# Performance work log

Hardware: AMD Instinct MI355X
Metric: run time of the kernel (lower is better)

## Reference

```python
import jax, jax.numpy as jnp
import numpy as np


def setup_inputs() -> dict:
    key = jax.random.key(0)
    kq, kk, kv = jax.random.split(key, 3)
    N, L, H, D = 2, 2048, 16, 64
    Q = jax.random.normal(kq, (N, L, H, D), dtype=jnp.float32)
    K = jax.random.normal(kk, (N, L, H, D), dtype=jnp.float32)
    V = jax.random.normal(kv, (N, L, H, D), dtype=jnp.float32)
    return {"Q": Q, "K": K, "V": V}


def reference(Q, K, V):
    # Q: [N, l_q, H, d], K: [N, l_k, H, d], V: [N, l_k, H, d_v]
    d_key = K.shape[-1]
    scale = 1.0 / jnp.sqrt(jnp.asarray(d_key, dtype=Q.dtype))
    # scores: [N, l_q, l_k, H] (matches torch sum over d, softmax over l_k)
    scores = jnp.einsum("nqhd,nkhd->nqkh", Q, K) * scale
    attn = jax.nn.softmax(scores, axis=2)
    # out: [N, l_q, H, d_v]
    out = jnp.einsum("nqkh,nkhd->nqhd", attn, V)
    return out
```

## Files before the change

### kernel.cpp

```cpp
#include <hip/hip_runtime.h>
#include <hip/hip_bf16.h>

typedef __attribute__((ext_vector_type(8))) short bf16x8;
typedef __attribute__((ext_vector_type(4))) float float4_t;
typedef __attribute__((ext_vector_type(2))) float f32x2;
typedef __attribute__((ext_vector_type(16))) float f32x16;
typedef __attribute__((ext_vector_type(4))) int int4v;
typedef __attribute__((ext_vector_type(2))) int int2v;
typedef __attribute__((ext_vector_type(4))) unsigned uint4v;

constexpr int Lseq = 2048;
constexpr int ROWS = 1024;
constexpr int KB   = 64;
constexpr float SCALE_LOG2E = 0.18033688011112042f;
constexpr float THR = 8.0f;

__device__ __forceinline__ int cvtpk(float lo, float hi) {
  int r; asm("v_cvt_pk_bf16_f32 %0, %1, %2" : "=v"(r) : "v"(lo), "v"(hi)); return r;
}
__device__ __forceinline__ f32x2 pkadd(f32x2 a, f32x2 b) {
  f32x2 r; asm("v_pk_add_f32 %0, %1, %2" : "=v"(r) : "v"(a), "v"(b)); return r;
}
__device__ __forceinline__ void plswap(int& a, int& b) {
  int2v r = __builtin_amdgcn_permlane32_swap(a, b, false, false);
  a = r[0]; b = r[1];
}
__device__ __forceinline__ float mx3(float a, float b, float c) {
  return fmaxf(fmaxf(a, b), c);
}
__device__ __forceinline__ int4v pk8(float4_t a, float4_t b) {
  int4v t;
  t[0] = cvtpk(a[0], a[1]); t[1] = cvtpk(a[2], a[3]);
  t[2] = cvtpk(b[0], b[1]); t[3] = cvtpk(b[2], b[3]);
  return t;
}
__device__ __forceinline__ uint4v make_srsrc(const void* p) {
  unsigned long long a = (unsigned long long)p;
  uint4v r; r[0] = (unsigned)a; r[1] = (unsigned)(a >> 32) & 0xffffu;
  r[2] = 0xffffffffu; r[3] = 0x00020000u;
  return r;
}
__device__ __forceinline__ float blds(unsigned voff, uint4v rs, int soff) {
  float d;
  asm volatile("buffer_load_dword %0, %1, %2, %3 offen"
               : "=v"(d) : "v"(voff), "s"(rs), "s"(soff));
  return d;
}

#define MFMA32(A, B, C) __builtin_amdgcn_mfma_f32_32x32x16_bf16((A), (B), (C), 0, 0, 0)

__global__ __launch_bounds__(256, 2)
void attn_fwd(const float* __restrict__ Qg, const float* __restrict__ Kg,
              const float* __restrict__ Vg, float* __restrict__ Og) {
  __shared__ __align__(16) short kv_lds[2][2][KB * 64];

  int wg  = blockIdx.x;
  int swz = (wg & 7) * 64 + (wg >> 3);
  int nh  = swz >> 4;
  int qt  = swz & 15;
  const size_t base = (size_t)(nh >> 4) * Lseq * ROWS + (size_t)(nh & 15) * 64;

  const int tid  = threadIdx.x;
  const int lane = tid & 63;
  const int wid  = tid >> 6;
  const int lq   = lane & 31;
  const int hi   = lane >> 5;

  bf16x8 qf[4];
  {
    const float* qrow = Qg + base + (size_t)(qt * 128 + wid * 32 + lq) * ROWS + hi * 8;
#pragma unroll
    for (int c = 0; c < 4; ++c) {
      float4_t a = *(const float4_t*)(qrow + c * 16);
      float4_t b = *(const float4_t*)(qrow + c * 16 + 4);
#pragma unroll
      for (int j = 0; j < 4; ++j) { a[j] *= SCALE_LOG2E; b[j] *= SCALE_LOG2E; }
      qf[c] = __builtin_bit_cast(bf16x8, pk8(a, b));
    }
  }

  const uint4v rsK = make_srsrc(Kg + base);
  const uint4v rsV = make_srsrc(Vg + base);
  unsigned voffk  = (unsigned)(((tid >> 2) * ROWS + (tid & 3) * 16) * 4);
  unsigned voffv  = (unsigned)((((tid >> 6) * 8) * ROWS + (tid & 63)) * 4);
  unsigned voffv2 = voffv + 131072u;

  const int krow = tid >> 2;
  const int kwb  = krow * 128 + (tid & 3) * 32;
  const int kswz = (krow & 7) << 4;
  const int kb0  = kwb ^ kswz, kb1 = (kwb + 16) ^ kswz;
  const int vd   = tid & 63;
  const int vwb  = vd * 128 + (tid >> 6) * 16;
  const int vswz = (vd & 7) << 4;
  const int vb0  = vwb ^ vswz, vb1 = (vwb + 64) ^ vswz;
  const int rsw = (lq & 7) << 4;
  const int rb0 = lq * 128 + hi * 16;
  const int rb1 = (32 + lq) * 128 + hi * 16;

  float4_t kr[4]; float vr[16];
  auto stage_issue = [&]() {
    asm volatile(
        "buffer_load_dwordx4 %0, %4, %5, 0 offen\n\t"
        "buffer_load_dwordx4 %1, %4, %5, 0 offen offset:16\n\t"
        "buffer_load_dwordx4 %2, %4, %5, 0 offen offset:32\n\t"
        "buffer_load_dwordx4 %3, %4, %5, 0 offen offset:48"
        : "=v"(kr[0]), "=v"(kr[1]), "=v"(kr[2]), "=v"(kr[3])
        : "v"(voffk), "s"(rsK));
#pragma unroll
    for (int j = 0; j < 8; ++j) {
      vr[j]     = blds(voffv,  rsV, j * 4096);
      vr[8 + j] = blds(voffv2, rsV, j * 4096);
    }
    voffk += 262144u; voffv += 262144u; voffv2 += 262144u;
  };
  auto stage_write = [&](int buf) {
    asm volatile("s_waitcnt vmcnt(0)"
                 : "+v"(kr[0]), "+v"(kr[1]), "+v"(kr[2]), "+v"(kr[3]),
                   "+v"(vr[0]), "+v"(vr[1]), "+v"(vr[2]), "+v"(vr[3]),
                   "+v"(vr[4]), "+v"(vr[5]), "+v"(vr[6]), "+v"(vr[7]),
                   "+v"(vr[8]), "+v"(vr[9]), "+v"(vr[10]), "+v"(vr[11]),
                   "+v"(vr[12]), "+v"(vr[13]), "+v"(vr[14]), "+v"(vr[15]));
    char* kdst = (char*)&kv_lds[buf][0][0];
    *(int4v*)(kdst + kb0) = pk8(kr[0], kr[1]);
    *(int4v*)(kdst + kb1) = pk8(kr[2], kr[3]);
    char* vdst = (char*)&kv_lds[buf][1][0];
    int4v w0, w1;
    w0[0] = cvtpk(vr[0], vr[1]);   w0[1] = cvtpk(vr[2], vr[3]);
    w0[2] = cvtpk(vr[4], vr[5]);   w0[3] = cvtpk(vr[6], vr[7]);
    w1[0] = cvtpk(vr[8], vr[9]);   w1[1] = cvtpk(vr[10], vr[11]);
    w1[2] = cvtpk(vr[12], vr[13]); w1[3] = cvtpk(vr[14], vr[15]);
    *(int4v*)(vdst + vb0) = w0;
    *(int4v*)(vdst + vb1) = w1;
  };

  float m = 0.f, l = 0.f;
  f32x16 acc0, acc1;
#pragma unroll
  for (int r = 0; r < 16; ++r) { acc0[r] = 0.f; acc1[r] = 0.f; }

  stage_issue();
  stage_write(0);
  __syncthreads();

  int cur = 0;
  for (int kt = 0; kt < Lseq; kt += KB) {
    const bool more = (kt + KB) < Lseq;
    if (more) stage_issue();

    f32x16 s0, s1;
#pragma unroll
    for (int r = 0; r < 16; ++r) { s0[r] = -m; s1[r] = -m; }
    const char* kld = (const char*)&kv_lds[cur][0][0];
#pragma unroll
    for (int c = 0; c < 4; ++c) {
      bf16x8 ka = *(const bf16x8*)(kld + ((rb0 + c * 32) ^ rsw));
      s0 = MFMA32(ka, qf[c], s0);
    }
#pragma unroll
    for (int c = 0; c < 4; ++c) {
      bf16x8 ka = *(const bf16x8*)(kld + ((rb1 + c * 32) ^ rsw));
      s1 = MFMA32(ka, qf[c], s1);
    }

    float w0 = mx3(s0[0], s0[1], s0[2]);
    float w1 = mx3(s0[3], s0[4], s0[5]);
    float w2 = mx3(s0[6], s0[7], s0[8]);
    float w3 = mx3(s0[9], s0[10], s0[11]);
    float w4 = mx3(s0[12], s0[13], s0[14]);
    float w5 = mx3(s0[15], s1[0], s1[1]);
    float w6 = mx3(s1[2], s1[3], s1[4]);
    float w7 = mx3(s1[5], s1[6], s1[7]);
    float w8 = mx3(s1[8], s1[9], s1[10]);
    float w9 = mx3(s1[11], s1[12], s1[13]);
    float wa = fmaxf(s1[14], s1[15]);
    float x0 = mx3(w0, w1, w2);
    float x1 = mx3(w3, w4, w5);
    float x2 = mx3(w6, w7, w8);
    float x3 = mx3(w9, wa, x2);
    float pm = mx3(x0, x1, x3);
    {
      int a = __float_as_int(pm), b = a;
      plswap(a, b);
      pm = fmaxf(__int_as_float(a), __int_as_float(b));
    }

    if (__all(pm <= THR)) {
#pragma unroll
      for (int r = 0; r < 16; ++r) {
        s0[r] = __builtin_amdgcn_exp2f(s0[r]);
        s1[r] = __builtin_amdgcn_exp2f(s1[r]);
      }
    } else {
      float mn = fmaxf(pm, 0.f);
      m += mn;
      float f = __builtin_amdgcn_exp2f(-mn);
      l *= f;
#pragma unroll
      for (int r = 0; r < 16; ++r) {
        int qr = (r & 3) + 8 * (r >> 2) + 4 * hi;
        float fq = __shfl(f, qr);
        acc0[r] *= fq; acc1[r] *= fq;
      }
#pragma unroll
      for (int r = 0; r < 16; ++r) {
        s0[r] = __builtin_amdgcn_exp2f(s0[r] - mn);
        s1[r] = __builtin_amdgcn_exp2f(s1[r] - mn);
      }
    }

#define S2(v, i) (f32x2{(v)[2 * (i)], (v)[2 * (i) + 1]})
    {
      f32x2 u0 = pkadd(S2(s0, 0), S2(s0, 1));
      f32x2 u1 = pkadd(S2(s0, 2), S2(s0, 3));
      f32x2 u2 = pkadd(S2(s0, 4), S2(s0, 5));
      f32x2 u3 = pkadd(S2(s0, 6), S2(s0, 7));
      f32x2 u4 = pkadd(S2(s1, 0), S2(s1, 1));
      f32x2 u5 = pkadd(S2(s1, 2), S2(s1, 3));
      f32x2 u6 = pkadd(S2(s1, 4), S2(s1, 5));
      f32x2 u7 = pkadd(S2(s1, 6), S2(s1, 7));
      u0 = pkadd(u0, u1); u2 = pkadd(u2, u3);
      u4 = pkadd(u4, u5); u6 = pkadd(u6, u7);
      u0 = pkadd(u0, u2); u4 = pkadd(u4, u6);
      u0 = pkadd(u0, u4);
      float rs = u0[0] + u0[1];
      int a = __float_as_int(rs), b = a;
      plswap(a, b);
      l += __int_as_float(a) + __int_as_float(b);
    }
#undef S2

    bf16x8 pa[4];
#pragma unroll
    for (int c = 0; c < 4; ++c) {
      const f32x16& sv = (c < 2) ? s0 : s1;
      const int br = (c & 1) * 8;
      int t0 = cvtpk(sv[br + 0], sv[br + 1]);
      int t1 = cvtpk(sv[br + 2], sv[br + 3]);
      int t2 = cvtpk(sv[br + 4], sv[br + 5]);
      int t3 = cvtpk(sv[br + 6], sv[br + 7]);
      plswap(t0, t2);
      plswap(t1, t3);
      int4v t; t[0] = t0; t[1] = t1; t[2] = t2; t[3] = t3;
      pa[c] = __builtin_bit_cast(bf16x8, t);
    }

    const char* vld = (const char*)&kv_lds[cur][1][0];
#pragma unroll
    for (int c = 0; c < 4; ++c) {
      bf16x8 vb = *(const bf16x8*)(vld + ((rb0 + c * 32) ^ rsw));
      acc0 = MFMA32(pa[c], vb, acc0);
    }
#pragma unroll
    for (int c = 0; c < 4; ++c) {
      bf16x8 vb = *(const bf16x8*)(vld + ((rb1 + c * 32) ^ rsw));
      acc1 = MFMA32(pa[c], vb, acc1);
    }

    if (more) stage_write(cur ^ 1);
    __syncthreads();
    cur ^= 1;
  }

  float linv = 1.0f / l;
#pragma unroll
  for (int r = 0; r < 16; ++r) {
    int qr = (r & 3) + 8 * (r >> 2) + 4 * hi;
    float li = __shfl(linv, qr);
    float* orow = Og + base + (size_t)(qt * 128 + wid * 32 + qr) * ROWS;
    orow[lq]      = acc0[r] * li;
    orow[32 + lq] = acc1[r] * li;
  }
}

extern "C" void kernel_launch(void* const* d_in, const int* in_sizes, int n_in,
                              void* d_out, int out_size, void* d_ws, size_t ws_size,
                              hipStream_t stream) {
  const float* Q = (const float*)d_in[0];
  const float* K = (const float*)d_in[1];
  const float* V = (const float*)d_in[2];
  float* O = (float*)d_out;
  attn_fwd<<<dim3(512), dim3(256), 0, stream>>>(Q, K, V, O);
}
```

Measured before the change: 65.79 us.

## Pre-convert K/V to swizzled bf16 images and DMA them directly into LDS

Adds a preconv kernel that converts K and V to bf16 once per call, pre-swizzled into the exact LDS tile layout, and writes them to global scratch buffers. The attention kernel then streams those tiles straight into LDS with global_load_lds, so the per-workgroup fp32 loads, packing and LDS writes disappear. Workgroups shrink to 128 threads covering 64 query rows, doubling the grid. The cost is a second launch plus the round trip through the global scratch buffers, and each workgroup now loads K/V for only 64 query rows, so K/V reuse per workgroup halves.

```diff
diff --git a/kernel.cpp b/kernel.cpp
--- a/kernel.cpp
+++ b/kernel.cpp
@@ -7,13 +7,14 @@
 typedef __attribute__((ext_vector_type(16))) float f32x16;
 typedef __attribute__((ext_vector_type(4))) int int4v;
 typedef __attribute__((ext_vector_type(2))) int int2v;
-typedef __attribute__((ext_vector_type(4))) unsigned uint4v;
 
 constexpr int Lseq = 2048;
 constexpr int ROWS = 1024;
-constexpr int KB   = 64;
 constexpr float SCALE_LOG2E = 0.18033688011112042f;
 constexpr float THR = 8.0f;
+
+__device__ short g_Kb[32 * 32 * 4096];
+__device__ short g_Vb[32 * 32 * 4096];
 
 __device__ __forceinline__ int cvtpk(float lo, float hi) {
   int r; asm("v_cvt_pk_bf16_f32 %0, %1, %2" : "=v"(r) : "v"(lo), "v"(hi)); return r;
@@ -34,30 +35,63 @@
   t[2] = cvtpk(b[0], b[1]); t[3] = cvtpk(b[2], b[3]);
   return t;
 }
-__device__ __forceinline__ uint4v make_srsrc(const void* p) {
-  unsigned long long a = (unsigned long long)p;
-  uint4v r; r[0] = (unsigned)a; r[1] = (unsigned)(a >> 32) & 0xffffu;
-  r[2] = 0xffffffffu; r[3] = 0x00020000u;
-  return r;
-}
-__device__ __forceinline__ float blds(unsigned voff, uint4v rs, int soff) {
-  float d;
-  asm volatile("buffer_load_dword %0, %1, %2, %3 offen"
-               : "=v"(d) : "v"(voff), "s"(rs), "s"(soff));
-  return d;
+__device__ __forceinline__ void dma16(const void* g, void* l) {
+  __builtin_amdgcn_global_load_lds(
+      (const __attribute__((address_space(1))) void*)g,
+      (__attribute__((address_space(3))) void*)l, 16, 0, 0);
 }
 
 #define MFMA32(A, B, C) __builtin_amdgcn_mfma_f32_32x32x16_bf16((A), (B), (C), 0, 0, 0)
 
-__global__ __launch_bounds__(256, 2)
-void attn_fwd(const float* __restrict__ Qg, const float* __restrict__ Kg,
-              const float* __restrict__ Vg, float* __restrict__ Og) {
-  __shared__ __align__(16) short kv_lds[2][2][KB * 64];
-
-  int wg  = blockIdx.x;
-  int swz = (wg & 7) * 64 + (wg >> 3);
-  int nh  = swz >> 4;
-  int qt  = swz & 15;
+__global__ __launch_bounds__(256)
+void preconv(const float* __restrict__ Kg, const float* __restrict__ Vg) {
+  const int bid = blockIdx.x;
+  const int nh = bid >> 5;
+  const int kt = bid & 31;
+  const size_t base = (size_t)(nh >> 4) * Lseq * ROWS + (size_t)(nh & 15) * 64;
+  const int tid = threadIdx.x;
+  char* kimg = (char*)g_Kb + ((size_t)nh * 32 + kt) * 8192;
+  char* vimg = (char*)g_Vb + ((size_t)nh * 32 + kt) * 8192;
+
+  {
+    const int row = tid >> 2;
+    const float* src = Kg + base + (size_t)(kt * 64 + row) * ROWS + (tid & 3) * 16;
+    float4_t a = ((const float4_t*)src)[0];
+    float4_t b = ((const float4_t*)src)[1];
+    float4_t c = ((const float4_t*)src)[2];
+    float4_t d = ((const float4_t*)src)[3];
+    const int swz = (row & 7) << 4;
+    const int wb  = row * 128 + (tid & 3) * 32;
+    *(int4v*)(kimg + (wb ^ swz))        = pk8(a, b);
+    *(int4v*)(kimg + ((wb + 16) ^ swz)) = pk8(c, d);
+  }
+  {
+    const int d0 = tid & 63;
+    const int lb = tid >> 6;
+    const float* src = Vg + base + (size_t)(kt * 64 + lb * 16) * ROWS + d0;
+    float v[16];
+#pragma unroll
+    for (int j = 0; j < 16; ++j) v[j] = src[(size_t)j * ROWS];
+    int4v w0, w1;
+    w0[0] = cvtpk(v[0], v[1]);   w0[1] = cvtpk(v[2], v[3]);
+    w0[2] = cvtpk(v[4], v[5]);   w0[3] = cvtpk(v[6], v[7]);
+    w1[0] = cvtpk(v[8], v[9]);   w1[1] = cvtpk(v[10], v[11]);
+    w1[2] = cvtpk(v[12], v[13]); w1[3] = cvtpk(v[14], v[15]);
+    const int swz = (d0 & 7) << 4;
+    const int wb  = d0 * 128 + lb * 32;
+    *(int4v*)(vimg + (wb ^ swz))        = w0;
+    *(int4v*)(vimg + ((wb + 16) ^ swz)) = w1;
+  }
+}
+
+__global__ __launch_bounds__(128, 2)
+void attn_fwd(const float* __restrict__ Qg, float* __restrict__ Og) {
+  __shared__ __align__(16) short kv_lds[2][2][64 * 64];
+
+  const int wg  = blockIdx.x;
+  const int swz = (wg & 7) * 128 + (wg >> 3);
+  const int nh  = swz >> 5;
+  const int qt  = swz & 31;
   const size_t base = (size_t)(nh >> 4) * Lseq * ROWS + (size_t)(nh & 15) * 64;
 
   const int tid  = threadIdx.x;
@@ -68,7 +102,7 @@
 
   bf16x8 qf[4];
   {
-    const float* qrow = Qg + base + (size_t)(qt * 128 + wid * 32 + lq) * ROWS + hi * 8;
+    const float* qrow = Qg + base + (size_t)(qt * 64 + wid * 32 + lq) * ROWS + hi * 8;
 #pragma unroll
     for (int c = 0; c < 4; ++c) {
       float4_t a = *(const float4_t*)(qrow + c * 16);
@@ -79,73 +113,31 @@
     }
   }
 
-  const uint4v rsK = make_srsrc(Kg + base);
-  const uint4v rsV = make_srsrc(Vg + base);
-  unsigned voffk  = (unsigned)(((tid >> 2) * ROWS + (tid & 3) * 16) * 4);
-  unsigned voffv  = (unsigned)((((tid >> 6) * 8) * ROWS + (tid & 63)) * 4);
-  unsigned voffv2 = voffv + 131072u;
-
-  const int krow = tid >> 2;
-  const int kwb  = krow * 128 + (tid & 3) * 32;
-  const int kswz = (krow & 7) << 4;
-  const int kb0  = kwb ^ kswz, kb1 = (kwb + 16) ^ kswz;
-  const int vd   = tid & 63;
-  const int vwb  = vd * 128 + (tid >> 6) * 16;
-  const int vswz = (vd & 7) << 4;
-  const int vb0  = vwb ^ vswz, vb1 = (vwb + 64) ^ vswz;
+  const char* gsrc = (const char*)(wid == 0 ? g_Kb : g_Vb) + (size_t)nh * (32 * 8192)
+                     + lane * 16;
+  auto stage = [&](int buf, int t) {
+    const char* s = gsrc + (size_t)t * 8192;
+    char* d = (char*)&kv_lds[buf][wid][0];
+#pragma unroll
+    for (int i = 0; i < 8; ++i) dma16(s + i * 1024, d + i * 1024);
+  };
+
   const int rsw = (lq & 7) << 4;
   const int rb0 = lq * 128 + hi * 16;
   const int rb1 = (32 + lq) * 128 + hi * 16;
 
-  float4_t kr[4]; float vr[16];
-  auto stage_issue = [&]() {
-    asm volatile(
-        "buffer_load_dwordx4 %0, %4, %5, 0 offen\n\t"
-        "buffer_load_dwordx4 %1, %4, %5, 0 offen offset:16\n\t"
-        "buffer_load_dwordx4 %2, %4, %5, 0 offen offset:32\n\t"
-        "buffer_load_dwordx4 %3, %4, %5, 0 offen offset:48"
-        : "=v"(kr[0]), "=v"(kr[1]), "=v"(kr[2]), "=v"(kr[3])
-        : "v"(voffk), "s"(rsK));
-#pragma unroll
-    for (int j = 0; j < 8; ++j) {
-      vr[j]     = blds(voffv,  rsV, j * 4096);
-      vr[8 + j] = blds(voffv2, rsV, j * 4096);
-    }
-    voffk += 262144u; voffv += 262144u; voffv2 += 262144u;
-  };
-  auto stage_write = [&](int buf) {
-    asm volatile("s_waitcnt vmcnt(0)"
-                 : "+v"(kr[0]), "+v"(kr[1]), "+v"(kr[2]), "+v"(kr[3]),
-                   "+v"(vr[0]), "+v"(vr[1]), "+v"(vr[2]), "+v"(vr[3]),
-                   "+v"(vr[4]), "+v"(vr[5]), "+v"(vr[6]), "+v"(vr[7]),
-                   "+v"(vr[8]), "+v"(vr[9]), "+v"(vr[10]), "+v"(vr[11]),
-                   "+v"(vr[12]), "+v"(vr[13]), "+v"(vr[14]), "+v"(vr[15]));
-    char* kdst = (char*)&kv_lds[buf][0][0];
-    *(int4v*)(kdst + kb0) = pk8(kr[0], kr[1]);
-    *(int4v*)(kdst + kb1) = pk8(kr[2], kr[3]);
-    char* vdst = (char*)&kv_lds[buf][1][0];
-    int4v w0, w1;
-    w0[0] = cvtpk(vr[0], vr[1]);   w0[1] = cvtpk(vr[2], vr[3]);
-    w0[2] = cvtpk(vr[4], vr[5]);   w0[3] = cvtpk(vr[6], vr[7]);
-    w1[0] = cvtpk(vr[8], vr[9]);   w1[1] = cvtpk(vr[10], vr[11]);
-    w1[2] = cvtpk(vr[12], vr[13]); w1[3] = cvtpk(vr[14], vr[15]);
-    *(int4v*)(vdst + vb0) = w0;
-    *(int4v*)(vdst + vb1) = w1;
-  };
-
   float m = 0.f, l = 0.f;
   f32x16 acc0, acc1;
 #pragma unroll
   for (int r = 0; r < 16; ++r) { acc0[r] = 0.f; acc1[r] = 0.f; }
 
-  stage_issue();
-  stage_write(0);
+  stage(0, 0);
+  asm volatile("s_waitcnt vmcnt(0)" ::: "memory");
   __syncthreads();
 
   int cur = 0;
-  for (int kt = 0; kt < Lseq; kt += KB) {
-    const bool more = (kt + KB) < Lseq;
-    if (more) stage_issue();
+  for (int t = 0; t < 32; ++t) {
+    if (t < 31) stage(cur ^ 1, t + 1);
 
     f32x16 s0, s1;
 #pragma unroll
@@ -240,8 +232,8 @@
       int t3 = cvtpk(sv[br + 6], sv[br + 7]);
       plswap(t0, t2);
       plswap(t1, t3);
-      int4v t; t[0] = t0; t[1] = t1; t[2] = t2; t[3] = t3;
-      pa[c] = __builtin_bit_cast(bf16x8, t);
+      int4v tt; tt[0] = t0; tt[1] = t1; tt[2] = t2; tt[3] = t3;
+      pa[c] = __builtin_bit_cast(bf16x8, tt);
     }
 
     const char* vld = (const char*)&kv_lds[cur][1][0];
@@ -256,7 +248,7 @@
       acc1 = MFMA32(pa[c], vb, acc1);
     }
 
-    if (more) stage_write(cur ^ 1);
+    asm volatile("s_waitcnt vmcnt(0)" ::: "memory");
     __syncthreads();
     cur ^= 1;
   }
@@ -266,7 +258,7 @@
   for (int r = 0; r < 16; ++r) {
     int qr = (r & 3) + 8 * (r >> 2) + 4 * hi;
     float li = __shfl(linv, qr);
-    float* orow = Og + base + (size_t)(qt * 128 + wid * 32 + qr) * ROWS;
+    float* orow = Og + base + (size_t)(qt * 64 + wid * 32 + qr) * ROWS;
     orow[lq]      = acc0[r] * li;
     orow[32 + lq] = acc1[r] * li;
   }
@@ -279,5 +271,6 @@
   const float* K = (const float*)d_in[1];
   const float* V = (const float*)d_in[2];
   float* O = (float*)d_out;
-  attn_fwd<<<dim3(512), dim3(256), 0, stream>>>(Q, K, V, O);
-}
+  preconv<<<dim3(1024), dim3(256), 0, stream>>>(K, V);
+  attn_fwd<<<dim3(1024), dim3(128), 0, stream>>>(Q, O);
+}
```

After: 71.68 us. +9.0%, slower.
